# Performance work log

Hardware: AMD Instinct MI355X
Metric: run time of the kernel (lower is better)

The kernel has to match this reference:

```python
import jax, jax.numpy as jnp
import numpy as np

EPS = 1e-7  # K.epsilon()
NUM_ROUTING = 3

def squash(v, axis=-1):
    s = jnp.sum(jnp.square(v), axis=axis, keepdims=True)
    scale = s / (1.0 + s) / jnp.sqrt(s + EPS)
    return scale * v

def setup_inputs() -> dict:
    key = jax.random.key(0)
    k1, k2 = jax.random.split(key)
    B, J, I = 64, 2048, 16   # batch, input_num_capsule, input_dim_capsule
    K_, D = 32, 16           # num_capsule, dim_capsule
    inputs = jax.random.normal(k1, (B, J, I), dtype=jnp.float32)
    W = jax.random.normal(k2, (K_, J, D, I), dtype=jnp.float32) * 0.05
    return {"inputs": inputs, "W": W}

def reference(inputs, W):
    # inputs: [B, J, I]; W: [K, J, D, I]
    # inputs_hat[b,k,j,d] = sum_i inputs[b,j,i] * W[k,j,d,i]
    u_hat = jnp.einsum('bji,kjdi->bkjd', inputs, W)  # [B,K,J,D]
    B, K_, J, D = u_hat.shape
    b = jnp.zeros((B, K_, J), dtype=u_hat.dtype)
    for i in range(NUM_ROUTING):
        c = jax.nn.softmax(b, axis=1)                # softmax over num_capsule (dim=1)
        s = jnp.einsum('bkj,bkjd->bkd', c, u_hat)    # [B,K,D]
        outputs = squash(s)
        if i < NUM_ROUTING - 1:
            b = b + jnp.einsum('bkd,bkjd->bkj', outputs, u_hat)
    return jnp.concatenate([outputs, c], axis=-1)    # [B, K, D+J]
```

## Files before the change

kernel.cpp:

```cpp
#include <hip/hip_runtime.h>
#include <hip/hip_bf16.h>

#define B_ 64
#define J_ 2048
#define K_ 32
#define D_ 16
#define KD 512
#define NCH 256
#define JCR 8

typedef __attribute__((ext_vector_type(8))) short short8v;
typedef __attribute__((ext_vector_type(16))) float f32x16;

__device__ __forceinline__ float bf2f(unsigned int bits16) {
  unsigned int u = bits16 << 16;
  return __builtin_bit_cast(float, u);
}
__device__ __forceinline__ unsigned int cvtpk(float lo, float hi) {
  unsigned int r;
  asm("v_cvt_pk_bf16_f32 %0, %1, %2" : "=v"(r) : "v"(lo), "v"(hi));
  return r;
}
__device__ __forceinline__ f32x16 zero16() {
  f32x16 z;
#pragma unroll
  for (int i = 0; i < 16; ++i) z[i] = 0.f;
  return z;
}

__device__ __forceinline__ void x_to_lds(const float* __restrict__ inp,
                                         unsigned int* __restrict__ XT_lds,
                                         int j0, int t) {
  const int b = t >> 3, jj = t & 7;
  const float* src = inp + ((size_t)b * J_ + j0 + jj) * 16;
  const float4 v0 = ((const float4*)src)[0];
  const float4 v1 = ((const float4*)src)[1];
  const float4 v2 = ((const float4*)src)[2];
  const float4 v3 = ((const float4*)src)[3];
  unsigned int* dst = &XT_lds[(jj * 64 + b) * 8];
  dst[0] = cvtpk(v0.x, v0.y); dst[1] = cvtpk(v0.z, v0.w);
  dst[2] = cvtpk(v1.x, v1.y); dst[3] = cvtpk(v1.z, v1.w);
  dst[4] = cvtpk(v2.x, v2.y); dst[5] = cvtpk(v2.z, v2.w);
  dst[6] = cvtpk(v3.x, v3.y); dst[7] = cvtpk(v3.z, v3.w);
}

__global__ __launch_bounds__(512, 1) void k_R0W(const float* __restrict__ inp,
                                                const float* __restrict__ W,
                                                unsigned short* __restrict__ WB,
                                                unsigned int* __restrict__ spart_pk) {
  const int ch = blockIdx.x;
  const int t = threadIdx.x;
  const int wave = t >> 6, lane = t & 63;
  const int hi = lane >> 5, b31 = lane & 31;
  const int j0 = ch * JCR;

  __shared__ unsigned int XT_lds[JCR * 64 * 8];
  x_to_lds(inp, XT_lds, j0, t);
  __syncthreads();

  const float* wsrc = W + ((size_t)(4 * wave + (b31 >> 4)) * J_ + j0) * 256 +
                      (b31 & 15) * 16 + 8 * hi;
  unsigned short* wdst = WB + (size_t)j0 * 8192 + (4 * wave + (b31 >> 4)) * 256 +
                         (b31 & 15) * 16 + 8 * hi;
  const size_t qstep = (size_t)2 * J_ * 256;

  f32x16 acc[2][2];
#pragma unroll
  for (int q = 0; q < 2; ++q)
#pragma unroll
    for (int bt = 0; bt < 2; ++bt) acc[q][bt] = zero16();

  float4 wc[4];
#pragma unroll
  for (int q = 0; q < 2; ++q) {
    wc[2 * q]     = *(const float4*)(wsrc + (size_t)q * qstep);
    wc[2 * q + 1] = *(const float4*)(wsrc + (size_t)q * qstep + 4);
  }

  for (int jj = 0; jj < JCR; ++jj) {
    float4 wn[4];
    if (jj + 1 < JCR) {
#pragma unroll
      for (int q = 0; q < 2; ++q) {
        const float* ws2 = wsrc + (size_t)(jj + 1) * 256 + (size_t)q * qstep;
        wn[2 * q] = *(const float4*)ws2;
        wn[2 * q + 1] = *(const float4*)(ws2 + 4);
      }
    }
    const short8v xf0 = __builtin_bit_cast(short8v,
        *(const uint4*)&XT_lds[((size_t)jj * 64 + b31) * 8 + 4 * hi]);
    const short8v xf1 = __builtin_bit_cast(short8v,
        *(const uint4*)&XT_lds[((size_t)jj * 64 + 32 + b31) * 8 + 4 * hi]);
#pragma unroll
    for (int q = 0; q < 2; ++q) {
      uint4 wv;
      wv.x = cvtpk(wc[2 * q].x, wc[2 * q].y);
      wv.y = cvtpk(wc[2 * q].z, wc[2 * q].w);
      wv.z = cvtpk(wc[2 * q + 1].x, wc[2 * q + 1].y);
      wv.w = cvtpk(wc[2 * q + 1].z, wc[2 * q + 1].w);
      *(uint4*)(wdst + (size_t)jj * 8192 + q * 512) = wv;
      const short8v af = __builtin_bit_cast(short8v, wv);
      acc[q][0] = __builtin_amdgcn_mfma_f32_32x32x16_bf16(af, xf0, acc[q][0], 0, 0, 0);
      acc[q][1] = __builtin_amdgcn_mfma_f32_32x32x16_bf16(af, xf1, acc[q][1], 0, 0, 0);
    }
#pragma unroll
    for (int p = 0; p < 4; ++p) wc[p] = wn[p];
  }

  const float sc = 1.f / 32.f;
#pragma unroll
  for (int q = 0; q < 2; ++q) {
#pragma unroll
    for (int bt = 0; bt < 2; ++bt) {
      const int keven = 4 * wave + 2 * q;
      const int b = bt * 32 + b31;
      const float* a = (const float*)&acc[q][bt];
      unsigned int* se = spart_pk + (((size_t)b * NCH + ch) * 32 + keven) * 8 + 2 * hi;
      *(uint2*)se = make_uint2(cvtpk(a[0] * sc, a[1] * sc), cvtpk(a[2] * sc, a[3] * sc));
      *(uint2*)(se + 4) = make_uint2(cvtpk(a[4] * sc, a[5] * sc), cvtpk(a[6] * sc, a[7] * sc));
      unsigned int* so = se + 8;
      *(uint2*)so = make_uint2(cvtpk(a[8] * sc, a[9] * sc), cvtpk(a[10] * sc, a[11] * sc));
      *(uint2*)(so + 4) =
          make_uint2(cvtpk(a[12] * sc, a[13] * sc), cvtpk(a[14] * sc, a[15] * sc));
    }
  }
}

template <int MODE>
__global__ __launch_bounds__(512, 1) void k_R(const float* __restrict__ inp,
                                              const unsigned short* __restrict__ WB,
                                              const unsigned short* __restrict__ osB,
                                              unsigned int* __restrict__ spart_pk,
                                              float* __restrict__ outp) {
  const int ch = blockIdx.x;
  const int t = threadIdx.x;
  const int wave = t >> 6, lane = t & 63;
  const int kq = wave & 3, bt = wave >> 2;
  const int hi = lane >> 5, b31 = lane & 31;
  const int b = bt * 32 + b31;
  const int j0 = ch * JCR;

  __shared__ unsigned int XT_lds[JCR * 64 * 8];
  __shared__ float Sbuf[2 * 4 * 2 * 32];
  __shared__ float c_lds[(MODE == 2) ? 32 * 64 * 9 : 4];

  x_to_lds(inp, XT_lds, j0, t);

  uint4 os_pk[8];
  {
    const unsigned short* osb = osB + ((size_t)bt * 64 + lane) * 8 + (size_t)(8 * kq) * 1024;
#pragma unroll
    for (int kk = 0; kk < 8; ++kk) os_pk[kk] = *(const uint4*)(osb + (size_t)kk * 1024);
  }

  float acc[4][16];
#pragma unroll
  for (int q = 0; q < 4; ++q)
#pragma unroll
    for (int s = 0; s < 16; ++s) acc[q][s] = 0.f;

  const unsigned short* waBase =
      WB + (size_t)j0 * 8192 + (b31 >> 4) * 256 + (b31 & 15) * 16 + 8 * hi + (size_t)kq * 2048;

  uint4 a_cur[4];
#pragma unroll
  for (int q = 0; q < 4; ++q) a_cur[q] = *(const uint4*)(waBase + q * 512);
  __syncthreads();

  for (int jj = 0; jj < JCR; ++jj) {
    uint4 a_nxt[4];
    if (jj + 1 < JCR) {
#pragma unroll
      for (int q = 0; q < 4; ++q)
        a_nxt[q] = *(const uint4*)(waBase + (size_t)(jj + 1) * 8192 + q * 512);
    }
    const short8v xf = __builtin_bit_cast(short8v,
        *(const uint4*)&XT_lds[((size_t)jj * 64 + b) * 8 + 4 * hi]);

    f32x16 u[4];
#pragma unroll
    for (int q = 0; q < 4; ++q)
      u[q] = __builtin_amdgcn_mfma_f32_32x32x16_bf16(
          __builtin_bit_cast(short8v, a_cur[q]), xf, zero16(), 0, 0, 0);

    float ee[4], eo[4];
    float Sp = 0.f;
#pragma unroll
    for (int q = 0; q < 4; ++q) {
      const unsigned int* o0 = (const unsigned int*)&os_pk[2 * q];
      const unsigned int* o1 = (const unsigned int*)&os_pk[2 * q + 1];
      float pe = 0.f, po = 0.f;
#pragma unroll
      for (int s = 0; s < 8; ++s) {
        const unsigned int w0 = o0[s >> 1], w1 = o1[s >> 1];
        pe = fmaf(u[q][s], bf2f((s & 1) ? (w0 >> 16) : (w0 & 0xffffu)), pe);
        po = fmaf(u[q][8 + s], bf2f((s & 1) ? (w1 >> 16) : (w1 & 0xffffu)), po);
      }
      pe += __shfl_xor(pe, 32);
      po += __shfl_xor(po, 32);
      ee[q] = __expf(pe);
      eo[q] = __expf(po);
      Sp += ee[q] + eo[q];
    }
    if (hi == 0) Sbuf[((jj & 1) * 8 + kq * 2 + bt) * 32 + b31] = Sp;
    __syncthreads();
    const int sb = (jj & 1) * 8;
    const float S = Sbuf[(sb + 0 * 2 + bt) * 32 + b31] + Sbuf[(sb + 1 * 2 + bt) * 32 + b31] +
                    Sbuf[(sb + 2 * 2 + bt) * 32 + b31] + Sbuf[(sb + 3 * 2 + bt) * 32 + b31];
    const float rS = __builtin_amdgcn_rcpf(S);
#pragma unroll
    for (int q = 0; q < 4; ++q) {
      const float ce = ee[q] * rS, co = eo[q] * rS;
#pragma unroll
      for (int s = 0; s < 8; ++s) {
        acc[q][s] = fmaf(ce, u[q][s], acc[q][s]);
        acc[q][8 + s] = fmaf(co, u[q][8 + s], acc[q][8 + s]);
      }
      if constexpr (MODE == 2) {
        if (hi == 0) {
          const int k0 = 8 * kq + 2 * q;
          c_lds[((k0)*64 + b) * 9 + jj] = ce;
          c_lds[((k0 + 1) * 64 + b) * 9 + jj] = co;
        }
      }
    }
#pragma unroll
    for (int q = 0; q < 4; ++q) a_cur[q] = a_nxt[q];
  }

#pragma unroll
  for (int q = 0; q < 4; ++q) {
    const int keven = 8 * kq + 2 * q;
    unsigned int* se = spart_pk + (((size_t)b * NCH + ch) * 32 + keven) * 8 + 2 * hi;
    *(uint2*)se = make_uint2(cvtpk(acc[q][0], acc[q][1]), cvtpk(acc[q][2], acc[q][3]));
    *(uint2*)(se + 4) = make_uint2(cvtpk(acc[q][4], acc[q][5]), cvtpk(acc[q][6], acc[q][7]));
    unsigned int* so = se + 8;
    *(uint2*)so = make_uint2(cvtpk(acc[q][8], acc[q][9]), cvtpk(acc[q][10], acc[q][11]));
    *(uint2*)(so + 4) =
        make_uint2(cvtpk(acc[q][12], acc[q][13]), cvtpk(acc[q][14], acc[q][15]));
  }

  if constexpr (MODE == 2) {
    __syncthreads();
#pragma unroll
    for (int m = 0; m < 4; ++m) {
      const int r = m * 512 + t;
      const int k = r >> 6, bb = r & 63;
      const float* cr = &c_lds[r * 9];
      float* orow = outp + ((size_t)bb * K_ + k) * 2064 + 16 + j0;
      *(float4*)orow = make_float4(cr[0], cr[1], cr[2], cr[3]);
      *(float4*)(orow + 4) = make_float4(cr[4], cr[5], cr[6], cr[7]);
    }
  }
}

__global__ __launch_bounds__(256) void k_squash(const unsigned int* __restrict__ spart_pk,
                                                float* __restrict__ osum,
                                                unsigned short* __restrict__ osB,
                                                float* __restrict__ outp,
                                                int first, int final_) {
  const int t = threadIdx.x;
  const int wave = t >> 6, lane = t & 63;
  const int gw = blockIdx.x * 4 + wave;
  const int b = gw >> 5, k = gw & 31;
  const int h = lane & 7, pg = lane >> 3;
  float s0 = 0.f, s1 = 0.f;
#pragma unroll 8
  for (int p = pg; p < NCH; p += 8) {
    const unsigned int v = spart_pk[(((size_t)b * NCH + p) * 32 + k) * 8 + h];
    s0 += bf2f(v & 0xffffu);
    s1 += bf2f(v >> 16);
  }
  s0 += __shfl_xor(s0, 8);  s1 += __shfl_xor(s1, 8);
  s0 += __shfl_xor(s0, 16); s1 += __shfl_xor(s1, 16);
  s0 += __shfl_xor(s0, 32); s1 += __shfl_xor(s1, 32);
  float ss = s0 * s0 + s1 * s1;
  ss += __shfl_xor(ss, 1); ss += __shfl_xor(ss, 2); ss += __shfl_xor(ss, 4);
  const float scale = (ss / (1.f + ss)) * rsqrtf(ss + 1e-7f);
  const float ov0 = scale * s0, ov1 = scale * s1;
  if (final_) {
    if (pg == 0)
      *(float2*)(outp + ((size_t)b * K_ + k) * 2064 + 2 * h) = make_float2(ov0, ov1);
  } else {
    if (pg == 0) {
      float2 prev = make_float2(0.f, 0.f);
      if (!first) prev = *(const float2*)(osum + b * KD + k * 16 + 2 * h);
      const float ns0 = prev.x + ov0, ns1 = prev.y + ov1;
      *(float2*)(osum + b * KD + k * 16 + 2 * h) = make_float2(ns0, ns1);
      const int d0 = 2 * h;
      const int hi0 = (d0 >> 2) & 1;
      const int slot0 = (d0 & 3) + ((d0 >> 3) << 2);
      *(unsigned int*)(osB + (((size_t)k * 2 + (b >> 5)) * 64 + hi0 * 32 + (b & 31)) * 8 +
                       slot0) = cvtpk(ns0, ns1);
    }
  }
}

extern "C" void kernel_launch(void* const* d_in, const int* in_sizes, int n_in,
                              void* d_out, int out_size, void* d_ws, size_t ws_size,
                              hipStream_t stream) {
  const float* inp = (const float*)d_in[0];
  const float* W   = (const float*)d_in[1];
  float* outp = (float*)d_out;
  char* ws = (char*)d_ws;
  unsigned short* WB = (unsigned short*)ws;
  unsigned int* spart_pk = (unsigned int*)(ws + (size_t)33554432);
  float* osum = (float*)(ws + (size_t)33554432 + 16777216);
  unsigned short* osB = (unsigned short*)(ws + (size_t)33554432 + 16777216 + 131072);

  k_R0W<<<NCH, 512, 0, stream>>>(inp, W, WB, spart_pk);
  k_squash<<<B_ * K_ / 4, 256, 0, stream>>>(spart_pk, osum, osB, outp, 1, 0);
  k_R<1><<<NCH, 512, 0, stream>>>(inp, WB, osB, spart_pk, nullptr);
  k_squash<<<B_ * K_ / 4, 256, 0, stream>>>(spart_pk, osum, osB, outp, 0, 0);
  k_R<2><<<NCH, 512, 0, stream>>>(inp, WB, osB, spart_pk, outp);
  k_squash<<<B_ * K_ / 4, 256, 0, stream>>>(spart_pk, osum, osB, outp, 0, 1);
}
```

Baseline: 83.29 us.

## Cache packed bf16 inputs globally and use nontemporal loads for W and c output

The first routing kernel now writes its packed bf16 transposed input tile to a workspace buffer. The later routing kernels read that tile straight into registers with software prefetch, so they no longer redo the fp32 load, convert, LDS staging and barrier. The one-time fp32 W read and the final c-coefficient output stores become nontemporal to reduce cache pollution. The cost is an extra workspace buffer and an added global write in the first kernel.

```diff
diff --git a/kernel.cpp b/kernel.cpp
--- a/kernel.cpp
+++ b/kernel.cpp
@@ -11,6 +11,7 @@
 
 typedef __attribute__((ext_vector_type(8))) short short8v;
 typedef __attribute__((ext_vector_type(16))) float f32x16;
+typedef __attribute__((ext_vector_type(4))) float f32x4v;
 
 __device__ __forceinline__ float bf2f(unsigned int bits16) {
   unsigned int u = bits16 << 16;
@@ -27,26 +28,18 @@
   for (int i = 0; i < 16; ++i) z[i] = 0.f;
   return z;
 }
-
-__device__ __forceinline__ void x_to_lds(const float* __restrict__ inp,
-                                         unsigned int* __restrict__ XT_lds,
-                                         int j0, int t) {
-  const int b = t >> 3, jj = t & 7;
-  const float* src = inp + ((size_t)b * J_ + j0 + jj) * 16;
-  const float4 v0 = ((const float4*)src)[0];
-  const float4 v1 = ((const float4*)src)[1];
-  const float4 v2 = ((const float4*)src)[2];
-  const float4 v3 = ((const float4*)src)[3];
-  unsigned int* dst = &XT_lds[(jj * 64 + b) * 8];
-  dst[0] = cvtpk(v0.x, v0.y); dst[1] = cvtpk(v0.z, v0.w);
-  dst[2] = cvtpk(v1.x, v1.y); dst[3] = cvtpk(v1.z, v1.w);
-  dst[4] = cvtpk(v2.x, v2.y); dst[5] = cvtpk(v2.z, v2.w);
-  dst[6] = cvtpk(v3.x, v3.y); dst[7] = cvtpk(v3.z, v3.w);
+__device__ __forceinline__ f32x4v nt_load4(const float* p) {
+  return __builtin_nontemporal_load((const f32x4v*)p);
+}
+__device__ __forceinline__ void nt_store4(float* p, float a, float b, float c, float d) {
+  f32x4v v = {a, b, c, d};
+  __builtin_nontemporal_store(v, (f32x4v*)p);
 }
 
 __global__ __launch_bounds__(512, 1) void k_R0W(const float* __restrict__ inp,
                                                 const float* __restrict__ W,
                                                 unsigned short* __restrict__ WB,
+                                                unsigned int* __restrict__ XTg,
                                                 unsigned int* __restrict__ spart_pk) {
   const int ch = blockIdx.x;
   const int t = threadIdx.x;
@@ -55,8 +48,26 @@
   const int j0 = ch * JCR;
 
   __shared__ unsigned int XT_lds[JCR * 64 * 8];
-  x_to_lds(inp, XT_lds, j0, t);
+  {
+    const int b = t >> 3, jj = t & 7;
+    const float* src = inp + ((size_t)b * J_ + j0 + jj) * 16;
+    const float4 v0 = ((const float4*)src)[0];
+    const float4 v1 = ((const float4*)src)[1];
+    const float4 v2 = ((const float4*)src)[2];
+    const float4 v3 = ((const float4*)src)[3];
+    unsigned int* dst = &XT_lds[(jj * 64 + b) * 8];
+    dst[0] = cvtpk(v0.x, v0.y); dst[1] = cvtpk(v0.z, v0.w);
+    dst[2] = cvtpk(v1.x, v1.y); dst[3] = cvtpk(v1.z, v1.w);
+    dst[4] = cvtpk(v2.x, v2.y); dst[5] = cvtpk(v2.z, v2.w);
+    dst[6] = cvtpk(v3.x, v3.y); dst[7] = cvtpk(v3.z, v3.w);
+  }
   __syncthreads();
+  {
+    uint4* gbase = (uint4*)(XTg + (size_t)j0 * 512);
+    const uint4* lbase = (const uint4*)XT_lds;
+    gbase[t] = lbase[t];
+    gbase[t + 512] = lbase[t + 512];
+  }
 
   const float* wsrc = W + ((size_t)(4 * wave + (b31 >> 4)) * J_ + j0) * 256 +
                       (b31 & 15) * 16 + 8 * hi;
@@ -70,21 +81,21 @@
 #pragma unroll
     for (int bt = 0; bt < 2; ++bt) acc[q][bt] = zero16();
 
-  float4 wc[4];
+  f32x4v wc[4];
 #pragma unroll
   for (int q = 0; q < 2; ++q) {
-    wc[2 * q]     = *(const float4*)(wsrc + (size_t)q * qstep);
-    wc[2 * q + 1] = *(const float4*)(wsrc + (size_t)q * qstep + 4);
+    wc[2 * q]     = nt_load4(wsrc + (size_t)q * qstep);
+    wc[2 * q + 1] = nt_load4(wsrc + (size_t)q * qstep + 4);
   }
 
   for (int jj = 0; jj < JCR; ++jj) {
-    float4 wn[4];
+    f32x4v wn[4];
     if (jj + 1 < JCR) {
 #pragma unroll
       for (int q = 0; q < 2; ++q) {
         const float* ws2 = wsrc + (size_t)(jj + 1) * 256 + (size_t)q * qstep;
-        wn[2 * q] = *(const float4*)ws2;
-        wn[2 * q + 1] = *(const float4*)(ws2 + 4);
+        wn[2 * q] = nt_load4(ws2);
+        wn[2 * q + 1] = nt_load4(ws2 + 4);
       }
     }
     const short8v xf0 = __builtin_bit_cast(short8v,
@@ -94,10 +105,10 @@
 #pragma unroll
     for (int q = 0; q < 2; ++q) {
       uint4 wv;
-      wv.x = cvtpk(wc[2 * q].x, wc[2 * q].y);
-      wv.y = cvtpk(wc[2 * q].z, wc[2 * q].w);
-      wv.z = cvtpk(wc[2 * q + 1].x, wc[2 * q + 1].y);
-      wv.w = cvtpk(wc[2 * q + 1].z, wc[2 * q + 1].w);
+      wv.x = cvtpk(wc[2 * q][0], wc[2 * q][1]);
+      wv.y = cvtpk(wc[2 * q][2], wc[2 * q][3]);
+      wv.z = cvtpk(wc[2 * q + 1][0], wc[2 * q + 1][1]);
+      wv.w = cvtpk(wc[2 * q + 1][2], wc[2 * q + 1][3]);
       *(uint4*)(wdst + (size_t)jj * 8192 + q * 512) = wv;
       const short8v af = __builtin_bit_cast(short8v, wv);
       acc[q][0] = __builtin_amdgcn_mfma_f32_32x32x16_bf16(af, xf0, acc[q][0], 0, 0, 0);
@@ -127,7 +138,7 @@
 }
 
 template <int MODE>
-__global__ __launch_bounds__(512, 1) void k_R(const float* __restrict__ inp,
+__global__ __launch_bounds__(512, 1) void k_R(const unsigned int* __restrict__ XTg,
                                               const unsigned short* __restrict__ WB,
                                               const unsigned short* __restrict__ osB,
                                               unsigned int* __restrict__ spart_pk,
@@ -140,11 +151,8 @@
   const int b = bt * 32 + b31;
   const int j0 = ch * JCR;
 
-  __shared__ unsigned int XT_lds[JCR * 64 * 8];
   __shared__ float Sbuf[2 * 4 * 2 * 32];
   __shared__ float c_lds[(MODE == 2) ? 32 * 64 * 9 : 4];
-
-  x_to_lds(inp, XT_lds, j0, t);
 
   uint4 os_pk[8];
   {
@@ -161,21 +169,22 @@
 
   const unsigned short* waBase =
       WB + (size_t)j0 * 8192 + (b31 >> 4) * 256 + (b31 & 15) * 16 + 8 * hi + (size_t)kq * 2048;
-
-  uint4 a_cur[4];
+  const unsigned int* xBase = XTg + (size_t)j0 * 512 + b * 8 + 4 * hi;
+
+  uint4 a_cur[4], b_cur;
 #pragma unroll
   for (int q = 0; q < 4; ++q) a_cur[q] = *(const uint4*)(waBase + q * 512);
-  __syncthreads();
+  b_cur = *(const uint4*)xBase;
 
   for (int jj = 0; jj < JCR; ++jj) {
-    uint4 a_nxt[4];
+    uint4 a_nxt[4], b_nxt;
     if (jj + 1 < JCR) {
 #pragma unroll
       for (int q = 0; q < 4; ++q)
         a_nxt[q] = *(const uint4*)(waBase + (size_t)(jj + 1) * 8192 + q * 512);
-    }
-    const short8v xf = __builtin_bit_cast(short8v,
-        *(const uint4*)&XT_lds[((size_t)jj * 64 + b) * 8 + 4 * hi]);
+      b_nxt = *(const uint4*)(xBase + (size_t)(jj + 1) * 512);
+    }
+    const short8v xf = __builtin_bit_cast(short8v, b_cur);
 
     f32x16 u[4];
 #pragma unroll
@@ -226,6 +235,7 @@
     }
 #pragma unroll
     for (int q = 0; q < 4; ++q) a_cur[q] = a_nxt[q];
+    b_cur = b_nxt;
   }
 
 #pragma unroll
@@ -248,8 +258,8 @@
       const int k = r >> 6, bb = r & 63;
       const float* cr = &c_lds[r * 9];
       float* orow = outp + ((size_t)bb * K_ + k) * 2064 + 16 + j0;
-      *(float4*)orow = make_float4(cr[0], cr[1], cr[2], cr[3]);
-      *(float4*)(orow + 4) = make_float4(cr[4], cr[5], cr[6], cr[7]);
+      nt_store4(orow, cr[0], cr[1], cr[2], cr[3]);
+      nt_store4(orow + 4, cr[4], cr[5], cr[6], cr[7]);
     }
   }
 }
@@ -305,13 +315,14 @@
   char* ws = (char*)d_ws;
   unsigned short* WB = (unsigned short*)ws;
   unsigned int* spart_pk = (unsigned int*)(ws + (size_t)33554432);
-  float* osum = (float*)(ws + (size_t)33554432 + 16777216);
-  unsigned short* osB = (unsigned short*)(ws + (size_t)33554432 + 16777216 + 131072);
-
-  k_R0W<<<NCH, 512, 0, stream>>>(inp, W, WB, spart_pk);
+  float* osum = (float*)(ws + (size_t)50331648);
+  unsigned short* osB = (unsigned short*)(ws + (size_t)50331648 + 131072);
+  unsigned int* XTg = (unsigned int*)(ws + (size_t)50331648 + 131072 + 65536);
+
+  k_R0W<<<NCH, 512, 0, stream>>>(inp, W, WB, XTg, spart_pk);
   k_squash<<<B_ * K_ / 4, 256, 0, stream>>>(spart_pk, osum, osB, outp, 1, 0);
-  k_R<1><<<NCH, 512, 0, stream>>>(inp, WB, osB, spart_pk, nullptr);
+  k_R<1><<<NCH, 512, 0, stream>>>(XTg, WB, osB, spart_pk, nullptr);
   k_squash<<<B_ * K_ / 4, 256, 0, stream>>>(spart_pk, osum, osB, outp, 0, 0);
-  k_R<2><<<NCH, 512, 0, stream>>>(inp, WB, osB, spart_pk, outp);
+  k_R<2><<<NCH, 512, 0, stream>>>(XTg, WB, osB, spart_pk, outp);
   k_squash<<<B_ * K_ / 4, 256, 0, stream>>>(spart_pk, osum, osB, outp, 0, 1);
 }
```

Measured after the change: 113.1 us. 35.8% more time.
